# Kernel tuning notes

Hardware: AMD Instinct MI355X
Metric: run time of the kernel (lower is better)

Reference implementation:

```python
import jax, jax.numpy as jnp
import numpy as np

B, N, K = 8, 2048, 32
EPS = 1e-5


def _lrelu(x):
    return jnp.where(x >= 0, x, 0.2 * x)


def _bn(x, p):
    # inference BatchNorm; x: [B, C, ...], p: [4, C] = (gamma, beta, mean, var)
    g, b, m, v = p[0], p[1], p[2], p[3]
    shape = (1, -1) + (1,) * (x.ndim - 2)
    scale = g * jax.lax.rsqrt(v + EPS)
    return (x - m.reshape(shape)) * scale.reshape(shape) + b.reshape(shape)


def _group(x, k):
    # ops.group with xyz_or_feature='feature', feature_or_diff='diff'
    # x: [B, C, N] -> edge features [B, 2C, N, k] = cat(neighbor - center, center)
    xt = jnp.transpose(x, (0, 2, 1))  # [B, N, C]
    sq = jnp.sum(xt * xt, axis=-1)    # [B, N]
    dist = sq[:, :, None] - 2.0 * jnp.einsum('bnc,bmc->bnm', xt, xt) + sq[:, None, :]
    idx = jax.lax.top_k(-dist, k)[1]  # [B, N, k] nearest neighbors
    nbr = jax.vmap(lambda f, i: f[i])(xt, idx)  # [B, N, k, C]
    center = xt[:, :, None, :]
    edge = jnp.concatenate([nbr - center, jnp.broadcast_to(center, nbr.shape)], axis=-1)
    return jnp.transpose(edge, (0, 3, 1, 2))  # [B, 2C, N, k]


def _edgeconv(x, w1, bn1, w2, bn2, k):
    e = _group(x, k)
    h = _lrelu(_bn(jnp.einsum('oc,bcnk->bonk', w1, e), bn1))
    h = _lrelu(_bn(jnp.einsum('oc,bcnk->bonk', w2, h), bn2))
    return jnp.max(h, axis=-1)  # max over neighbors -> [B, C_out, N]


def _model(x,
           ec1_w1, ec1_bn1, ec1_w2, ec1_bn2,
           ec2_w1, ec2_bn1, ec2_w2, ec2_bn2,
           ec3_w1, ec3_bn1, ec3_w2, ec3_bn2,
           emb_w, q_w, k_w, v_w, att_bn1, ff_w1, ff_w2, att_bn2,
           cb_w, cb_bn):
    # EdgeConvBlock (3 stacked EdgeConvs, outputs concatenated)
    f1 = _edgeconv(x, ec1_w1, ec1_bn1, ec1_w2, ec1_bn2, K)
    f2 = _edgeconv(f1, ec2_w1, ec2_bn1, ec2_w2, ec2_bn2, K)
    f3 = _edgeconv(f2, ec3_w1, ec3_bn1, ec3_w2, ec3_bn2, K)
    xc = jnp.concatenate([f1, f2, f3], axis=1)  # [B, 192, N]
    # Point2PointAttentionBlock: embedding then dense self-attention
    h = jnp.einsum('oc,bcn->bon', emb_w, xc)  # [B, 1024, N]
    q = jnp.einsum('oc,bcn->bon', q_w, h)
    kk = jnp.einsum('oc,bcn->bon', k_w, h)
    v = jnp.einsum('oc,bcn->bon', v_w, h)
    scale = jnp.sqrt(jnp.asarray(h.shape[1], h.dtype))
    att = jax.nn.softmax(jnp.einsum('bcn,bcm->bnm', q, kk) / scale, axis=-1)  # [B, N, N]
    x_r = jnp.einsum('bnm,bcm->bcn', att, v)
    h = _bn(h + x_r, att_bn1)
    ff = jnp.einsum('oc,bcn->bon', ff_w2, _lrelu(jnp.einsum('oc,bcn->bon', ff_w1, h)))
    h = _bn(h + ff, att_bn2)
    # ConvBlock head
    return _lrelu(_bn(jnp.einsum('oc,bcn->bon', cb_w, h), cb_bn))  # [B, 1024, N]


def setup_inputs() -> dict:
    key = jax.random.key(0)
    ks = iter(jax.random.split(key, 32))

    def randn(shape, s=0.1):
        return jax.random.normal(next(ks), shape, jnp.float32) * s

    def bnp(c):
        return jax.random.uniform(next(ks), (4, c), jnp.float32, 0.1, 1.0)

    return {
        'x': randn((B, 3, N), 1.0),
        'ec1_w1': randn((64, 6)), 'ec1_bn1': bnp(64),
        'ec1_w2': randn((64, 64)), 'ec1_bn2': bnp(64),
        'ec2_w1': randn((64, 128)), 'ec2_bn1': bnp(64),
        'ec2_w2': randn((64, 64)), 'ec2_bn2': bnp(64),
        'ec3_w1': randn((64, 128)), 'ec3_bn1': bnp(64),
        'ec3_w2': randn((64, 64)), 'ec3_bn2': bnp(64),
        'emb_w': randn((1024, 192), 0.05),
        'q_w': randn((1024, 1024), 0.03),
        'k_w': randn((1024, 1024), 0.03),
        'v_w': randn((1024, 1024), 0.03),
        'att_bn1': bnp(1024),
        'ff_w1': randn((512, 1024), 0.03),
        'ff_w2': randn((1024, 512), 0.03),
        'att_bn2': bnp(1024),
        'cb_w': randn((1024, 1024), 0.03),
        'cb_bn': bnp(1024),
    }


def reference(x,
              ec1_w1, ec1_bn1, ec1_w2, ec1_bn2,
              ec2_w1, ec2_bn1, ec2_w2, ec2_bn2,
              ec3_w1, ec3_bn1, ec3_w2, ec3_bn2,
              emb_w, q_w, k_w, v_w, att_bn1, ff_w1, ff_w2, att_bn2,
              cb_w, cb_bn):
    return _model(x,
                  ec1_w1, ec1_bn1, ec1_w2, ec1_bn2,
                  ec2_w1, ec2_bn1, ec2_w2, ec2_bn2,
                  ec3_w1, ec3_bn1, ec3_w2, ec3_bn2,
                  emb_w, q_w, k_w, v_w, att_bn1, ff_w1, ff_w2, att_bn2,
                  cb_w, cb_bn)
```

## Files before the change

kernel.cpp:

```cpp
#include <hip/hip_runtime.h>
#include <hip/hip_bf16.h>

constexpr int Bn  = 8;
constexpr int Np  = 2048;
constexpr int KNN = 32;

typedef __attribute__((ext_vector_type(8))) short bf16x8;
typedef __attribute__((ext_vector_type(4))) float f32x4;

__device__ static inline void gll16(const void* g, void* l) {
  __builtin_amdgcn_global_load_lds((const __attribute__((address_space(1))) void*)g,
                                   (__attribute__((address_space(3))) void*)l, 16, 0, 0);
}

__device__ static inline unsigned short f2bf(float x) {
  union { __hip_bfloat16 h; unsigned short u; } cv; cv.h = __float2bfloat16(x); return cv.u;
}
__device__ static inline float bf2f(unsigned short u) {
  union { __hip_bfloat16 h; unsigned short u; } cv; cv.u = u; return __bfloat162float(cv.h);
}

__global__ __launch_bounds__(256)
void cvt_bf16_kernel(const float* __restrict__ s, __hip_bfloat16* __restrict__ d, int n) {
  int i = blockIdx.x * 256 + threadIdx.x;
  if (i < n) d[i] = __float2bfloat16(s[i]);
}

template<int CIN, int K1>
__global__ __launch_bounds__(256)
void cvt_w1a(const float* __restrict__ w1, __hip_bfloat16* __restrict__ out) {
  int i = blockIdx.x * 256 + threadIdx.x;
  if (i >= 64 * K1) return;
  int o = i / K1, c = i - o * K1;
  out[i] = __float2bfloat16(c < CIN ? w1[o * 2 * CIN + c] : 0.f);
}

__global__ __launch_bounds__(256)
void xpose_kernel(const float* __restrict__ x, float* __restrict__ xt,
                  __hip_bfloat16* __restrict__ xb) {
  int i = blockIdx.x * 256 + threadIdx.x;
  int b = i >> 11, n = i & 2047;
  const float* p = x + (long)b * 3 * Np + n;
  float vx = p[0], vy = p[Np], vz = p[2 * Np];
  xt[(long)i * 4 + 0] = vx;
  xt[(long)i * 4 + 1] = vy;
  xt[(long)i * 4 + 2] = vz;
  xt[(long)i * 4 + 3] = 0.f;
  __hip_bfloat16* q = xb + (long)i * 8;
  q[0] = __float2bfloat16(vx); q[1] = __float2bfloat16(vy);
  q[2] = __float2bfloat16(vz);
  q[3] = __float2bfloat16(0.f); q[4] = q[3]; q[5] = q[3]; q[6] = q[3]; q[7] = q[3];
}

template<int C, int CP>
__global__ __launch_bounds__(256)
void sq_kernel(const float* __restrict__ f, float* __restrict__ out) {
  int i = blockIdx.x * 256 + threadIdx.x;
  const float* p = f + (long)i * CP;
  float s = 0.f;
#pragma unroll
  for (int c = 0; c < C; ++c) s += p[c] * p[c];
  out[i] = s;
}

template<int CIN, int CP>
__global__ __launch_bounds__(256)
void split_kernel(const float* __restrict__ f, __hip_bfloat16* __restrict__ fhi,
                  __hip_bfloat16* __restrict__ flo) {
  int i = blockIdx.x * 256 + threadIdx.x;
  int n = i >> 6, c = i & 63;
  float v = (c < CIN) ? f[(long)n * CP + c] : 0.f;
  __hip_bfloat16 h = __float2bfloat16(v);
  fhi[i] = h;
  flo[i] = __float2bfloat16(v - __bfloat162float(h));
}

__device__ static inline unsigned umin32(unsigned a, unsigned b) { return a < b ? a : b; }

__device__ static inline unsigned long long shfl64x(unsigned long long k, int m) {
  unsigned lo = (unsigned)__shfl_xor((int)(unsigned)k, m);
  unsigned hi = (unsigned)__shfl_xor((int)(unsigned)(k >> 32), m);
  return ((unsigned long long)hi << 32) | (unsigned long long)lo;
}

__device__ static inline unsigned lane_sort64_u32(unsigned v, int lane) {
#pragma unroll
  for (int k = 2; k <= 64; k <<= 1) {
#pragma unroll
    for (int j = k >> 1; j > 0; j >>= 1) {
      unsigned o = (unsigned)__shfl_xor((int)v, j);
      bool dir = ((lane & k) == 0);
      bool lower = ((lane & j) == 0);
      bool keep = (v < o) == (dir == lower);
      v = keep ? v : o;
    }
  }
  return v;
}

__device__ static inline unsigned long long lane_sort64_u64(unsigned long long v, int lane) {
#pragma unroll
  for (int k = 2; k <= 64; k <<= 1) {
#pragma unroll
    for (int j = k >> 1; j > 0; j >>= 1) {
      unsigned long long o = shfl64x(v, j);
      bool dir = ((lane & k) == 0);
      bool lower = ((lane & j) == 0);
      bool keep = (v < o) == (dir == lower);
      v = keep ? v : o;
    }
  }
  return v;
}

__device__ static inline unsigned long long lane_merge64(unsigned long long a,
                                                         unsigned long long b, int lane) {
  unsigned long long br = shfl64x(b, 63);
  unsigned long long m = a < br ? a : br;
#pragma unroll
  for (int j = 32; j > 0; j >>= 1) {
    unsigned long long o = shfl64x(m, j);
    bool lower = ((lane & j) == 0);
    bool keep = (m < o) == lower;
    m = keep ? m : o;
  }
  return m;
}

template<int MAP, int CAP>
__device__ static inline void row_topk(const unsigned* val, unsigned long long* cbuf,
                                       int lane, int* outp) {
  unsigned tmn[16];
#pragma unroll
  for (int i = 0; i < 16; ++i) tmn[i] = umin32(val[i], val[i + 16]);
#pragma unroll
  for (int w2 = 8; w2 >= 1; w2 >>= 1)
#pragma unroll
    for (int i = 0; i < 8; ++i)
      if (i < w2) tmn[i] = umin32(tmn[i], tmn[i + w2]);

  unsigned T = (unsigned)__shfl((int)lane_sort64_u32(tmn[0], lane), 31);

  int S = 0;
#pragma unroll
  for (int s = 0; s < 32; ++s) {
    bool p = val[s] <= T;
    unsigned long long mask = __ballot(p);
    int pre = __builtin_amdgcn_mbcnt_hi((unsigned)(mask >> 32),
              __builtin_amdgcn_mbcnt_lo((unsigned)mask, 0u));
    int pos = S + pre;
    unsigned idx = (MAP == 0) ? (unsigned)((s >> 2) * 256 + lane * 4 + (s & 3))
                              : (unsigned)((s >> 2) * 256 + (s & 3) * 64 + lane);
    if (p && pos < CAP) cbuf[pos] = ((unsigned long long)val[s] << 32) | idx;
    S += (int)__popcll(mask);
  }

  unsigned long long cur;
  if (S <= CAP) {
    unsigned long long k0 = (lane < S) ? cbuf[lane] : ~0ull;
    cur = lane_sort64_u64(k0, lane);
    for (int c = 64; c < S; c += 64) {
      unsigned long long kc = (c + lane < S) ? cbuf[c + lane] : ~0ull;
      cur = lane_merge64(cur, lane_sort64_u64(kc, lane), lane);
    }
  } else {
    cur = ~0ull;
    for (int s = 0; s < 32; ++s) {
      unsigned idx = (MAP == 0) ? (unsigned)((s >> 2) * 256 + lane * 4 + (s & 3))
                                : (unsigned)((s >> 2) * 256 + (s & 3) * 64 + lane);
      unsigned long long kc = ((unsigned long long)val[s] << 32) | idx;
      cur = lane_merge64(cur, lane_sort64_u64(kc, lane), lane);
    }
  }
  if (lane < KNN) outp[lane] = (int)(unsigned)cur;
}

__global__ __launch_bounds__(512)
void knn3_kernel(const float* __restrict__ xt, const float* __restrict__ sqb,
                 int* __restrict__ idxOut) {
  __shared__ float4 F[2048];
  __shared__ float sqS[2048];
  __shared__ unsigned long long cbuf[8 * 256];
  int t = threadIdx.x, lane = t & 63, w = t >> 6;
  long pb = (long)blockIdx.y * Np;
  for (int e = t; e < 2048; e += 512) {
    F[e] = ((const float4*)xt)[pb + e];
    sqS[e] = sqb[pb + e];
  }
  __syncthreads();
  int row = blockIdx.x * 8 + w;
  float4 a = F[row];
  unsigned val[32];
#pragma unroll
  for (int j4 = 0; j4 < 8; ++j4)
#pragma unroll
    for (int u = 0; u < 4; ++u) {
      int col = j4 * 256 + u * 64 + lane;
      float4 fb = F[col];
      float d = sqS[col] - 2.f * (a.x * fb.x + a.y * fb.y + a.z * fb.z);
      unsigned b = __float_as_uint(d);
      val[j4 * 4 + u] = b ^ ((unsigned)((int)b >> 31) | 0x80000000u);
    }
  row_topk<1, 256>(val, cbuf + w * 256, lane, idxOut + (pb + row) * KNN);
}

__global__ __launch_bounds__(512, 4)
void knn16_kernel(const __hip_bfloat16* __restrict__ fhi,
                  const __hip_bfloat16* __restrict__ flo,
                  const float* __restrict__ sqb, int* __restrict__ idxOut) {
  constexpr int LDW = 2052;
  constexpr int CAP = 224;
  __shared__ __align__(16) float Dw[8 * LDW];
  __shared__ unsigned long long cbuf[8 * CAP];
  int t = threadIdx.x, lane = t & 63, w = t >> 6;
  long pb = (long)blockIdx.y * Np;
  int r0 = blockIdx.x * 8;
  const __hip_bfloat16* fh = fhi + pb * 64;
  const __hip_bfloat16* fl = flo + pb * 64;
  const float* sqg = sqb + pb;

  int ar = r0 + (lane & 7);
  int kc = (lane >> 4) * 8;
  int n15 = lane & 15;
  bf16x8 ah[2], al[2];
#pragma unroll
  for (int k2 = 0; k2 < 2; ++k2) {
    ah[k2] = *(const bf16x8*)(fh + (long)ar * 64 + k2 * 32 + kc);
    al[k2] = *(const bf16x8*)(fl + (long)ar * 64 + k2 * 32 + kc);
  }

  int cb0 = w * 256;
  bf16x8 b0h[2], b0l[2], b1h[2], b1l[2];
  float sq0, sq1;
  {
    int bc = cb0 + n15;
#pragma unroll
    for (int k2 = 0; k2 < 2; ++k2) {
      b0h[k2] = *(const bf16x8*)(fh + (long)bc * 64 + k2 * 32 + kc);
      b0l[k2] = *(const bf16x8*)(fl + (long)bc * 64 + k2 * 32 + kc);
    }
    sq0 = sqg[bc];
    bc = cb0 + 16 + n15;
#pragma unroll
    for (int k2 = 0; k2 < 2; ++k2) {
      b1h[k2] = *(const bf16x8*)(fh + (long)bc * 64 + k2 * 32 + kc);
      b1l[k2] = *(const bf16x8*)(fl + (long)bc * 64 + k2 * 32 + kc);
    }
    sq1 = sqg[bc];
  }
  int m0 = (lane >> 4) * 4;
  bool wr = (lane < 32);
#pragma unroll
  for (int cp = 0; cp < 8; ++cp) {
    {
      int ct = cp * 2;
      bf16x8 nh[2], nl[2]; float nsq = 0.f;
      if (ct + 2 < 16) {
        int bc = cb0 + (ct + 2) * 16 + n15;
#pragma unroll
        for (int k2 = 0; k2 < 2; ++k2) {
          nh[k2] = *(const bf16x8*)(fh + (long)bc * 64 + k2 * 32 + kc);
          nl[k2] = *(const bf16x8*)(fl + (long)bc * 64 + k2 * 32 + kc);
        }
        nsq = sqg[bc];
      }
      f32x4 acc = f32x4{0.f, 0.f, 0.f, 0.f};
#pragma unroll
      for (int k2 = 0; k2 < 2; ++k2) {
        acc = __builtin_amdgcn_mfma_f32_16x16x32_bf16(ah[k2], b0h[k2], acc, 0, 0, 0);
        acc = __builtin_amdgcn_mfma_f32_16x16x32_bf16(ah[k2], b0l[k2], acc, 0, 0, 0);
        acc = __builtin_amdgcn_mfma_f32_16x16x32_bf16(al[k2], b0h[k2], acc, 0, 0, 0);
      }
      if (wr) {
        int col = cb0 + ct * 16 + n15;
#pragma unroll
        for (int r = 0; r < 4; ++r)
          Dw[(m0 + r) * LDW + col] = sq0 - 2.f * acc[r];
      }
#pragma unroll
      for (int k2 = 0; k2 < 2; ++k2) { b0h[k2] = nh[k2]; b0l[k2] = nl[k2]; }
      sq0 = nsq;
    }
    {
      int ct = cp * 2 + 1;
      bf16x8 nh[2], nl[2]; float nsq = 0.f;
      if (ct + 2 < 16) {
        int bc = cb0 + (ct + 2) * 16 + n15;
#pragma unroll
        for (int k2 = 0; k2 < 2; ++k2) {
          nh[k2] = *(const bf16x8*)(fh + (long)bc * 64 + k2 * 32 + kc);
          nl[k2] = *(const bf16x8*)(fl + (long)bc * 64 + k2 * 32 + kc);
        }
        nsq = sqg[bc];
      }
      f32x4 acc = f32x4{0.f, 0.f, 0.f, 0.f};
#pragma unroll
      for (int k2 = 0; k2 < 2; ++k2) {
        acc = __builtin_amdgcn_mfma_f32_16x16x32_bf16(ah[k2], b1h[k2], acc, 0, 0, 0);
        acc = __builtin_amdgcn_mfma_f32_16x16x32_bf16(ah[k2], b1l[k2], acc, 0, 0, 0);
        acc = __builtin_amdgcn_mfma_f32_16x16x32_bf16(al[k2], b1h[k2], acc, 0, 0, 0);
      }
      if (wr) {
        int col = cb0 + ct * 16 + n15;
#pragma unroll
        for (int r = 0; r < 4; ++r)
          Dw[(m0 + r) * LDW + col] = sq1 - 2.f * acc[r];
      }
#pragma unroll
      for (int k2 = 0; k2 < 2; ++k2) { b1h[k2] = nh[k2]; b1l[k2] = nl[k2]; }
      sq1 = nsq;
    }
  }
  __syncthreads();

  {
    unsigned val[32];
    const float4* rp = (const float4*)&Dw[w * LDW];
#pragma unroll
    for (int j4 = 0; j4 < 8; ++j4) {
      float4 f4 = rp[j4 * 64 + lane];
      float fv[4] = {f4.x, f4.y, f4.z, f4.w};
#pragma unroll
      for (int u = 0; u < 4; ++u) {
        unsigned b = __float_as_uint(fv[u]);
        val[j4 * 4 + u] = b ^ ((unsigned)((int)b >> 31) | 0x80000000u);
      }
    }
    row_topk<0, CAP>(val, cbuf + w * CAP, lane, idxOut + (pb + r0 + w) * KNN);
  }
}

template<int CIN, int CP>
__global__ __launch_bounds__(256)
void biasker(const float* __restrict__ feat, const float* __restrict__ w1,
             float* __restrict__ bias) {
  __shared__ float wd[64][CIN + 1];
  int tid = threadIdx.x;
  for (int e = tid; e < 64 * CIN; e += 256) {
    int o = e / CIN, c = e - o * CIN;
    wd[o][c] = w1[o * 2 * CIN + CIN + c] - w1[o * 2 * CIN + c];
  }
  __syncthreads();
  int wv = tid >> 6, o = tid & 63;
  float wr_[CIN];
#pragma unroll
  for (int c = 0; c < CIN; ++c) wr_[c] = wd[o][c];
  long base = (long)blockIdx.y * Np + blockIdx.x * 32 + wv * 8;
  for (int p = 0; p < 8; ++p) {
    const float* fr = feat + (base + p) * CP;
    float acc = 0.f;
#pragma unroll
    for (int c = 0; c < CIN; ++c) acc = fmaf(wr_[c], fr[c], acc);
    bias[(base + p) * 64 + o] = acc;
  }
}

template<int K1>
__global__ __launch_bounds__(256)
void edge_mfma(const __hip_bfloat16* __restrict__ featb, int fstride,
               const int* __restrict__ idx, const float* __restrict__ bias,
               const __hip_bfloat16* __restrict__ w1b,
               const __hip_bfloat16* __restrict__ w2b,
               const float* __restrict__ bn1, const float* __restrict__ bn2,
               float* __restrict__ fout, __hip_bfloat16* __restrict__ xcseg) {
  __shared__ __align__(16) char lds[32768 + 64 * K1 * 2 + 8192 + 1024 + 512];
  __hip_bfloat16* A  = (__hip_bfloat16*)lds;
  __hip_bfloat16* H1 = A + 128 * K1;
  float*          H2 = (float*)lds;
  __hip_bfloat16* W1 = (__hip_bfloat16*)(lds + 32768);
  __hip_bfloat16* W2 = W1 + 64 * K1;
  float* biasS = (float*)(lds + 32768 + 64 * K1 * 2 + 8192);
  int*   idxS  = (int*)(biasS + 256);

  int t = threadIdx.x, lane = t & 63, w = t >> 6;
  long pb = (long)blockIdx.y * Np;
  int p0 = blockIdx.x * 4;

  if (t < 128) idxS[t] = idx[(pb + p0 + (t >> 5)) * KNN + (t & 31)];
  biasS[w * 64 + lane] = bias[(pb + p0 + w) * 64 + lane];
  for (int e = t; e < 64 * K1 / 8; e += 256)
    ((ulonglong2*)W1)[e] = ((const ulonglong2*)w1b)[e];
  for (int e = t; e < 512; e += 256)
    ((ulonglong2*)W2)[e] = ((const ulonglong2*)w2b)[e];
  __syncthreads();

  if (K1 == 64) {
#pragma unroll
    for (int i = 0; i < 4; ++i) {
      int e = t + i * 256;
      int r = e >> 3, cc = e & 7;
      const ulonglong2* src = (const ulonglong2*)(featb + (pb + idxS[r]) * fstride) + cc;
      ((ulonglong2*)(A + r * 64))[cc] = *src;
    }
  } else {
    if (t < 128) {
      int r = t;
      ulonglong2 z; z.x = 0; z.y = 0;
      ((ulonglong2*)(A + r * 32))[0] = *(const ulonglong2*)(featb + (pb + idxS[r]) * fstride);
      ((ulonglong2*)(A + r * 32))[1] = z;
      ((ulonglong2*)(A + r * 32))[2] = z;
      ((ulonglong2*)(A + r * 32))[3] = z;
    }
  }

  int ocol = lane & 15;
  float sc1[4], sh1[4], sc2[4], sh2[4];
#pragma unroll
  for (int jn = 0; jn < 4; ++jn) {
    int o = jn * 16 + ocol;
    sc1[jn] = bn1[o] * rsqrtf(bn1[192 + o] + 1e-5f);
    sh1[jn] = bn1[64 + o] - bn1[128 + o] * sc1[jn];
    sc2[jn] = bn2[o] * rsqrtf(bn2[192 + o] + 1e-5f);
    sh2[jn] = bn2[64 + o] - bn2[128 + o] * sc2[jn];
  }
  __syncthreads();

  int mrow = lane & 15;
  int kc   = (lane >> 4) * 8;
  constexpr int KS = K1 / 32;

  f32x4 acc[2][4];
#pragma unroll
  for (int im = 0; im < 2; ++im)
#pragma unroll
    for (int jn = 0; jn < 4; ++jn) acc[im][jn] = f32x4{0.f, 0.f, 0.f, 0.f};
#pragma unroll
  for (int s = 0; s < KS; ++s) {
    bf16x8 af[2], bf_[4];
#pragma unroll
    for (int im = 0; im < 2; ++im)
      af[im] = *(const bf16x8*)(A + (w * 32 + im * 16 + mrow) * K1 + s * 32 + kc);
#pragma unroll
    for (int jn = 0; jn < 4; ++jn)
      bf_[jn] = *(const bf16x8*)(W1 + (jn * 16 + mrow) * K1 + s * 32 + kc);
#pragma unroll
    for (int im = 0; im < 2; ++im)
#pragma unroll
      for (int jn = 0; jn < 4; ++jn)
        acc[im][jn] = __builtin_amdgcn_mfma_f32_16x16x32_bf16(af[im], bf_[jn], acc[im][jn], 0, 0, 0);
  }
#pragma unroll
  for (int im = 0; im < 2; ++im)
#pragma unroll
    for (int jn = 0; jn < 4; ++jn) {
      int o = jn * 16 + ocol;
      float bsv = biasS[w * 64 + o];
#pragma unroll
      for (int r = 0; r < 4; ++r) {
        int m = w * 32 + im * 16 + (lane >> 4) * 4 + r;
        float x = (acc[im][jn][r] + bsv) * sc1[jn] + sh1[jn];
        x = fmaxf(x, 0.2f * x);
        H1[m * 64 + o] = __float2bfloat16(x);
      }
    }
  __syncthreads();

  bf16x8 a2[2][2], b2[4][2];
#pragma unroll
  for (int im = 0; im < 2; ++im)
#pragma unroll
    for (int s = 0; s < 2; ++s)
      a2[im][s] = *(const bf16x8*)(H1 + (w * 32 + im * 16 + mrow) * 64 + s * 32 + kc);
#pragma unroll
  for (int jn = 0; jn < 4; ++jn)
#pragma unroll
    for (int s = 0; s < 2; ++s)
      b2[jn][s] = *(const bf16x8*)(W2 + (jn * 16 + mrow) * 64 + s * 32 + kc);
  __syncthreads();

  f32x4 acc2[2][4];
#pragma unroll
  for (int im = 0; im < 2; ++im)
#pragma unroll
    for (int jn = 0; jn < 4; ++jn) acc2[im][jn] = f32x4{0.f, 0.f, 0.f, 0.f};
#pragma unroll
  for (int s = 0; s < 2; ++s)
#pragma unroll
    for (int im = 0; im < 2; ++im)
#pragma unroll
      for (int jn = 0; jn < 4; ++jn)
        acc2[im][jn] = __builtin_amdgcn_mfma_f32_16x16x32_bf16(a2[im][s], b2[jn][s], acc2[im][jn], 0, 0, 0);
#pragma unroll
  for (int im = 0; im < 2; ++im)
#pragma unroll
    for (int jn = 0; jn < 4; ++jn) {
      int o = jn * 16 + ocol;
#pragma unroll
      for (int r = 0; r < 4; ++r) {
        int m = w * 32 + im * 16 + (lane >> 4) * 4 + r;
        float x = acc2[im][jn][r] * sc2[jn] + sh2[jn];
        x = fmaxf(x, 0.2f * x);
        H2[m * 64 + o] = x;
      }
    }
  __syncthreads();

  {
    int o = t & 63;
    float m = -3.4e38f;
#pragma unroll
    for (int k = 0; k < 32; ++k) m = fmaxf(m, H2[(w * 32 + k) * 64 + o]);
    int n2 = p0 + w;
    if (fout) fout[(pb + n2) * 64 + o] = m;
    xcseg[(pb + n2) * 192 + o] = __float2bfloat16(m);
  }
}

template<int OUTF, int BNMODE, int RESID, int LRELU>
__global__ __launch_bounds__(512)
void gemm_db(const __hip_bfloat16* __restrict__ A, int lda, long sA,
             const __hip_bfloat16* __restrict__ B, int ldb, long sB,
             void* __restrict__ Cv, int ldc, long sC,
             const __hip_bfloat16* __restrict__ R, long sR,
             const float* __restrict__ bn, int bnlen, int Kd,
             int gx, int gy) {
  int nwg = gx * gy * Bn;
  int cpx = nwg >> 3;
  int orig = blockIdx.x;
  int wg = (orig & 7) * cpx + (orig >> 3);
  int bz = wg / (gx * gy);
  int rem = wg - bz * (gx * gy);
  int by = rem / gx;
  int bx = rem - by * gx;
  A += (long)bz * sA;
  B += (long)bz * sB;
  long i0 = (long)bx * 256, j0 = (long)by * 256;

  __shared__ __hip_bfloat16 As[2][256 * 64];
  __shared__ __hip_bfloat16 Bs[2][256 * 64];

  int t = threadIdx.x, lane = t & 63, w = t >> 6;
  int wm = w & 1, wn = w >> 1;

  f32x4 acc[8][4];
#pragma unroll
  for (int im = 0; im < 8; ++im)
#pragma unroll
    for (int jn = 0; jn < 4; ++jn) acc[im][jn] = f32x4{0.f, 0.f, 0.f, 0.f};

#define STAGE_DB(bi, kt)                                                     \
  {                                                                          \
    _Pragma("unroll")                                                        \
    for (int i = 0; i < 4; ++i) {                                            \
      int e = t + i * 512;                                                   \
      int r = e >> 3, c = e & 7;                                             \
      int cs = c ^ (r & 7);                                                  \
      gll16(A + (i0 + r) * lda + (kt) * 64 + cs * 8,                         \
            (__hip_bfloat16*)As[bi] + e * 8);                                \
    }                                                                        \
    _Pragma("unroll")                                                        \
    for (int i = 0; i < 4; ++i) {                                            \
      int e = t + i * 512;                                                   \
      int r = e >> 3, c = e & 7;                                             \
      int cs = c ^ (r & 7);                                                  \
      gll16(B + (j0 + r) * ldb + (kt) * 64 + cs * 8,                         \
            (__hip_bfloat16*)Bs[bi] + e * 8);                                \
    }                                                                        \
  }

  int nt = Kd >> 6;
  STAGE_DB(0, 0);
  __syncthreads();

  int cur = 0;
  for (int kt = 0; kt < nt; ++kt) {
    if (kt + 1 < nt) STAGE_DB(cur ^ 1, kt + 1);
    const __hip_bfloat16* Ab = As[cur];
    const __hip_bfloat16* Bb = Bs[cur];
#pragma unroll
    for (int ks = 0; ks < 2; ++ks) {
      bf16x8 af[8], bfv[4];
#pragma unroll
      for (int im = 0; im < 8; ++im) {
        int ra = wm * 128 + im * 16 + (lane & 15);
        int q = (ks * 4 + (lane >> 4)) ^ (ra & 7);
        af[im] = *(const bf16x8*)(Ab + ra * 64 + q * 8);
      }
#pragma unroll
      for (int jn = 0; jn < 4; ++jn) {
        int rb = wn * 64 + jn * 16 + (lane & 15);
        int q = (ks * 4 + (lane >> 4)) ^ (rb & 7);
        bfv[jn] = *(const bf16x8*)(Bb + rb * 64 + q * 8);
      }
#pragma unroll
      for (int im = 0; im < 8; ++im)
#pragma unroll
        for (int jn = 0; jn < 4; ++jn)
          acc[im][jn] = __builtin_amdgcn_mfma_f32_16x16x32_bf16(af[im], bfv[jn], acc[im][jn], 0, 0, 0);
    }
    __syncthreads();
    cur ^= 1;
  }
#undef STAGE_DB

  int mlocal = (lane >> 4) * 4;
  int nlocal = lane & 15;
#pragma unroll
  for (int i = 0; i < 8; ++i) {
    long m0 = i0 + wm * 128 + i * 16 + mlocal;
    float bsc[4], bsh[4];
    if (BNMODE == 1) {
#pragma unroll
      for (int r = 0; r < 4; ++r) {
        long c = m0 + r;
        float sc = bn[c] * rsqrtf(bn[3 * bnlen + c] + 1e-5f);
        bsc[r] = sc;
        bsh[r] = bn[bnlen + c] - bn[2 * bnlen + c] * sc;
      }
    }
#pragma unroll
    for (int j = 0; j < 4; ++j) {
      long nn = j0 + wn * 64 + j * 16 + nlocal;
      float sc2 = 1.f, sh2 = 0.f;
      if (BNMODE == 2) {
        sc2 = bn[nn] * rsqrtf(bn[3 * bnlen + nn] + 1e-5f);
        sh2 = bn[bnlen + nn] - bn[2 * bnlen + nn] * sc2;
      }
      f32x4 v = acc[i][j];
      float o4[4];
      ushort4 rv;
      if (RESID) rv = *(const ushort4*)(R + (long)bz * sR + nn * ldc + m0);
#pragma unroll
      for (int r = 0; r < 4; ++r) {
        float x = v[r];
        if (RESID) x += bf2f(r == 0 ? rv.x : r == 1 ? rv.y : r == 2 ? rv.z : rv.w);
        if (BNMODE == 1) x = x * bsc[r] + bsh[r];
        if (BNMODE == 2) x = x * sc2 + sh2;
        if (LRELU) x = (x >= 0.f) ? x : 0.2f * x;
        o4[r] = x;
      }
      if (OUTF) {
        float* Cp = (float*)Cv + (long)bz * sC + nn * ldc + m0;
        *(float4*)Cp = make_float4(o4[0], o4[1], o4[2], o4[3]);
      } else {
        __hip_bfloat16* Cp = (__hip_bfloat16*)Cv + (long)bz * sC + nn * ldc + m0;
        ushort4 sv;
        sv.x = f2bf(o4[0]); sv.y = f2bf(o4[1]); sv.z = f2bf(o4[2]); sv.w = f2bf(o4[3]);
        *(ushort4*)Cp = sv;
      }
    }
  }
}

__global__ __launch_bounds__(256)
void softmax_bf(__hip_bfloat16* __restrict__ S) {
  long row = (long)blockIdx.y * Np + blockIdx.x;
  __hip_bfloat16* p = S + row * Np;
  int t = threadIdx.x;
  const float scale = 0.03125f;
  float v[8];
  float mx = -3.4e38f;
#pragma unroll
  for (int u = 0; u < 8; ++u) {
    v[u] = __bfloat162float(p[u * 256 + t]) * scale;
    mx = fmaxf(mx, v[u]);
  }
  __shared__ float red[4];
#pragma unroll
  for (int off = 32; off > 0; off >>= 1) mx = fmaxf(mx, __shfl_xor(mx, off));
  if ((t & 63) == 0) red[t >> 6] = mx;
  __syncthreads();
  mx = fmaxf(fmaxf(red[0], red[1]), fmaxf(red[2], red[3]));
  __syncthreads();
  float sum = 0.f;
#pragma unroll
  for (int u = 0; u < 8; ++u) { v[u] = __expf(v[u] - mx); sum += v[u]; }
#pragma unroll
  for (int off = 32; off > 0; off >>= 1) sum += __shfl_xor(sum, off);
  if ((t & 63) == 0) red[t >> 6] = sum;
  __syncthreads();
  sum = red[0] + red[1] + red[2] + red[3];
  float inv = 1.f / sum;
#pragma unroll
  for (int u = 0; u < 8; ++u) p[u * 256 + t] = __float2bfloat16(v[u] * inv);
}

extern "C" void kernel_launch(void* const* d_in, const int* in_sizes, int n_in,
                              void* d_out, int out_size, void* d_ws, size_t ws_size,
                              hipStream_t stream) {
  const float* x       = (const float*)d_in[0];
  const float* ec1_w1  = (const float*)d_in[1];
  const float* ec1_bn1 = (const float*)d_in[2];
  const float* ec1_w2  = (const float*)d_in[3];
  const float* ec1_bn2 = (const float*)d_in[4];
  const float* ec2_w1  = (const float*)d_in[5];
  const float* ec2_bn1 = (const float*)d_in[6];
  const float* ec2_w2  = (const float*)d_in[7];
  const float* ec2_bn2 = (const float*)d_in[8];
  const float* ec3_w1  = (const float*)d_in[9];
  const float* ec3_bn1 = (const float*)d_in[10];
  const float* ec3_w2  = (const float*)d_in[11];
  const float* ec3_bn2 = (const float*)d_in[12];
  const float* emb_w   = (const float*)d_in[13];
  const float* q_w     = (const float*)d_in[14];
  const float* k_w     = (const float*)d_in[15];
  const float* v_w     = (const float*)d_in[16];
  const float* att_bn1 = (const float*)d_in[17];
  const float* ff_w1   = (const float*)d_in[18];
  const float* ff_w2   = (const float*)d_in[19];
  const float* att_bn2 = (const float*)d_in[20];
  const float* cb_w    = (const float*)d_in[21];
  const float* cb_bn   = (const float*)d_in[22];
  float* out = (float*)d_out;
  (void)in_sizes; (void)n_in; (void)out_size; (void)ws_size;

  float* ws  = (float*)d_ws;
  float* xt  = ws;
  float* f1  = xt + 65536;
  float* f2  = f1 + 1048576;
  float* sqb = f2 + 1048576;
  int*   idxb = (int*)(sqb + 16384);
  __hip_bfloat16* xc  = (__hip_bfloat16*)(idxb + 524288);
  __hip_bfloat16* wts = xc + 3145728;
  __hip_bfloat16* ew  = wts + 5439488;
  __hip_bfloat16* xb  = ew + 22528;
  float* big = (float*)(xb + 131072);
  __hip_bfloat16* hb  = (__hip_bfloat16*)big;
  __hip_bfloat16* qb  = hb + 16777216;
  __hip_bfloat16* kb  = qb + 16777216;
  __hip_bfloat16* vtb = kb + 16777216;
  __hip_bfloat16* Sb  = vtb + 16777216;
  __hip_bfloat16* fhi = (__hip_bfloat16*)big;
  __hip_bfloat16* flo = fhi + 1048576;
  float* biasb = big + 33554432;

  __hip_bfloat16* emb_wb = wts;
  __hip_bfloat16* q_wb   = wts + 196608;
  __hip_bfloat16* k_wb   = wts + 1245184;
  __hip_bfloat16* v_wb   = wts + 2293760;
  __hip_bfloat16* ff1_wb = wts + 3342336;
  __hip_bfloat16* ff2_wb = wts + 3866624;
  __hip_bfloat16* cb_wb  = wts + 4390912;

  __hip_bfloat16* w1a1_b = ew;
  __hip_bfloat16* w2_1b  = ew + 2048;
  __hip_bfloat16* w1a2_b = ew + 6144;
  __hip_bfloat16* w2_2b  = ew + 10240;
  __hip_bfloat16* w1a3_b = ew + 14336;
  __hip_bfloat16* w2_3b  = ew + 18432;

  const long sN1024 = (long)Np * 1024;
  const long sN512  = (long)Np * 512;
  const long sN192  = (long)Np * 192;
  const long sNN    = (long)Np * Np;

  cvt_bf16_kernel<<<768,  256, 0, stream>>>(emb_w, emb_wb, 196608);
  cvt_bf16_kernel<<<4096, 256, 0, stream>>>(q_w,   q_wb,   1048576);
  cvt_bf16_kernel<<<4096, 256, 0, stream>>>(k_w,   k_wb,   1048576);
  cvt_bf16_kernel<<<4096, 256, 0, stream>>>(v_w,   v_wb,   1048576);
  cvt_bf16_kernel<<<2048, 256, 0, stream>>>(ff_w1, ff1_wb, 524288);
  cvt_bf16_kernel<<<2048, 256, 0, stream>>>(ff_w2, ff2_wb, 524288);
  cvt_bf16_kernel<<<4096, 256, 0, stream>>>(cb_w,  cb_wb,  1048576);
  cvt_w1a<3, 32><<<8, 256, 0, stream>>>(ec1_w1, w1a1_b);
  cvt_w1a<64, 64><<<16, 256, 0, stream>>>(ec2_w1, w1a2_b);
  cvt_w1a<64, 64><<<16, 256, 0, stream>>>(ec3_w1, w1a3_b);
  cvt_bf16_kernel<<<16, 256, 0, stream>>>(ec1_w2, w2_1b, 4096);
  cvt_bf16_kernel<<<16, 256, 0, stream>>>(ec2_w2, w2_2b, 4096);
  cvt_bf16_kernel<<<16, 256, 0, stream>>>(ec3_w2, w2_3b, 4096);

  xpose_kernel<<<64, 256, 0, stream>>>(x, xt, xb);

  sq_kernel<3, 4><<<64, 256, 0, stream>>>(xt, sqb);
  knn3_kernel<<<dim3(Np / 8, Bn), 512, 0, stream>>>(xt, sqb, idxb);
  biasker<3, 4><<<dim3(Np / 32, Bn), 256, 0, stream>>>(xt, ec1_w1, biasb);
  edge_mfma<32><<<dim3(Np / 4, Bn), 256, 0, stream>>>(
      xb, 8, idxb, biasb, w1a1_b, w2_1b, ec1_bn1, ec1_bn2, f1, xc);

  sq_kernel<64, 64><<<64, 256, 0, stream>>>(f1, sqb);
  split_kernel<64, 64><<<4096, 256, 0, stream>>>(f1, fhi, flo);
  knn16_kernel<<<dim3(Np / 8, Bn), 512, 0, stream>>>(fhi, flo, sqb, idxb);
  biasker<64, 64><<<dim3(Np / 32, Bn), 256, 0, stream>>>(f1, ec2_w1, biasb);
  edge_mfma<64><<<dim3(Np / 4, Bn), 256, 0, stream>>>(
      xc, 192, idxb, biasb, w1a2_b, w2_2b, ec2_bn1, ec2_bn2, f2, xc + 64);

  sq_kernel<64, 64><<<64, 256, 0, stream>>>(f2, sqb);
  split_kernel<64, 64><<<4096, 256, 0, stream>>>(f2, fhi, flo);
  knn16_kernel<<<dim3(Np / 8, Bn), 512, 0, stream>>>(fhi, flo, sqb, idxb);
  biasker<64, 64><<<dim3(Np / 32, Bn), 256, 0, stream>>>(f2, ec3_w1, biasb);
  edge_mfma<64><<<dim3(Np / 4, Bn), 256, 0, stream>>>(
      xc + 64, 192, idxb, biasb, w1a3_b, w2_3b, ec3_bn1, ec3_bn2, nullptr, xc + 128);

  gemm_db<0, 0, 0, 0><<<dim3(4 * 8 * Bn), 512, 0, stream>>>(
      emb_wb, 192, 0, xc, 192, sN192, hb, 1024, sN1024, nullptr, 0, nullptr, 0, 192, 4, 8);

  gemm_db<0, 0, 0, 0><<<dim3(4 * 8 * Bn), 512, 0, stream>>>(
      q_wb, 1024, 0, hb, 1024, sN1024, qb, 1024, sN1024, nullptr, 0, nullptr, 0, 1024, 4, 8);
  gemm_db<0, 0, 0, 0><<<dim3(4 * 8 * Bn), 512, 0, stream>>>(
      k_wb, 1024, 0, hb, 1024, sN1024, kb, 1024, sN1024, nullptr, 0, nullptr, 0, 1024, 4, 8);
  gemm_db<0, 0, 0, 0><<<dim3(8 * 4 * Bn), 512, 0, stream>>>(
      hb, 1024, sN1024, v_wb, 1024, 0, vtb, 2048, sN1024, nullptr, 0, nullptr, 0, 1024, 8, 4);

  gemm_db<0, 0, 0, 0><<<dim3(8 * 8 * Bn), 512, 0, stream>>>(
      kb, 1024, sN1024, qb, 1024, sN1024, Sb, 2048, sNN, nullptr, 0, nullptr, 0, 1024, 8, 8);
  softmax_bf<<<dim3(Np, Bn), 256, 0, stream>>>(Sb);

  gemm_db<0, 1, 1, 0><<<dim3(4 * 8 * Bn), 512, 0, stream>>>(
      vtb, 2048, sN1024, Sb, 2048, sNN, hb, 1024, sN1024, hb, sN1024, att_bn1, 1024, 2048, 4, 8);

  gemm_db<0, 0, 0, 1><<<dim3(2 * 8 * Bn), 512, 0, stream>>>(
      ff1_wb, 1024, 0, hb, 1024, sN1024, qb, 512, sN512, nullptr, 0, nullptr, 0, 1024, 2, 8);
  gemm_db<0, 1, 1, 0><<<dim3(4 * 8 * Bn), 512, 0, stream>>>(
      ff2_wb, 512, 0, qb, 512, sN512, hb, 1024, sN1024, hb, sN1024, att_bn2, 1024, 512, 4, 8);

  gemm_db<1, 2, 0, 1><<<dim3(8 * 4 * Bn), 512, 0, stream>>>(
      hb, 1024, sN1024, cb_wb, 1024, 0, out, 2048, sN1024, nullptr, 0, cb_bn, 1024, 1024, 8, 4);
}
```

Before: 1.012 ms.

## Replace bitonic top-k sorts with radix-select and double kNN rows per block

Swaps the bitonic sort used to find the 32nd-smallest threshold and the final candidate sort for a bitwise radix-select that uses wave ballots and popcounts. The selected indices are written unsorted through mbcnt compaction. The knn16 kernel now handles 16 rows per block instead of 8, so all MFMA output lanes are used, and it stages the squared norms in LDS instead of loading them per column. Risks include the changed output order of neighbor indices, if downstream code depends on it, plus larger LDS use and lower occupancy in knn16.

```diff
diff --git a/kernel.cpp b/kernel.cpp
--- a/kernel.cpp
+++ b/kernel.cpp
@@ -77,25 +77,15 @@
 
 __device__ static inline unsigned umin32(unsigned a, unsigned b) { return a < b ? a : b; }
 
+__device__ static inline int mbcnt64(unsigned long long m) {
+  return __builtin_amdgcn_mbcnt_hi((unsigned)(m >> 32),
+         __builtin_amdgcn_mbcnt_lo((unsigned)m, 0u));
+}
+
 __device__ static inline unsigned long long shfl64x(unsigned long long k, int m) {
   unsigned lo = (unsigned)__shfl_xor((int)(unsigned)k, m);
   unsigned hi = (unsigned)__shfl_xor((int)(unsigned)(k >> 32), m);
   return ((unsigned long long)hi << 32) | (unsigned long long)lo;
-}
-
-__device__ static inline unsigned lane_sort64_u32(unsigned v, int lane) {
-#pragma unroll
-  for (int k = 2; k <= 64; k <<= 1) {
-#pragma unroll
-    for (int j = k >> 1; j > 0; j >>= 1) {
-      unsigned o = (unsigned)__shfl_xor((int)v, j);
-      bool dir = ((lane & k) == 0);
-      bool lower = ((lane & j) == 0);
-      bool keep = (v < o) == (dir == lower);
-      v = keep ? v : o;
-    }
-  }
-  return v;
 }
 
 __device__ static inline unsigned long long lane_sort64_u64(unsigned long long v, int lane) {
@@ -127,6 +117,16 @@
   return m;
 }
 
+__device__ static inline unsigned kth_u32(unsigned v, int km1) {
+  unsigned p = 0;
+#pragma unroll
+  for (int b = 31; b >= 0; --b) {
+    unsigned t = p | (1u << b);
+    if ((int)__popcll(__ballot(v < t)) <= km1) p = t;
+  }
+  return p;
+}
+
 template<int MAP, int CAP>
 __device__ static inline void row_topk(const unsigned* val, unsigned long long* cbuf,
                                        int lane, int* outp) {
@@ -139,40 +139,81 @@
     for (int i = 0; i < 8; ++i)
       if (i < w2) tmn[i] = umin32(tmn[i], tmn[i + w2]);
 
-  unsigned T = (unsigned)__shfl((int)lane_sort64_u32(tmn[0], lane), 31);
+  unsigned T = kth_u32(tmn[0], 31);
 
   int S = 0;
 #pragma unroll
   for (int s = 0; s < 32; ++s) {
     bool p = val[s] <= T;
     unsigned long long mask = __ballot(p);
-    int pre = __builtin_amdgcn_mbcnt_hi((unsigned)(mask >> 32),
-              __builtin_amdgcn_mbcnt_lo((unsigned)mask, 0u));
-    int pos = S + pre;
+    int pos = S + mbcnt64(mask);
     unsigned idx = (MAP == 0) ? (unsigned)((s >> 2) * 256 + lane * 4 + (s & 3))
                               : (unsigned)((s >> 2) * 256 + (s & 3) * 64 + lane);
     if (p && pos < CAP) cbuf[pos] = ((unsigned long long)val[s] << 32) | idx;
     S += (int)__popcll(mask);
   }
 
-  unsigned long long cur;
-  if (S <= CAP) {
-    unsigned long long k0 = (lane < S) ? cbuf[lane] : ~0ull;
-    cur = lane_sort64_u64(k0, lane);
-    for (int c = 64; c < S; c += 64) {
-      unsigned long long kc = (c + lane < S) ? cbuf[c + lane] : ~0ull;
-      cur = lane_merge64(cur, lane_sort64_u64(kc, lane), lane);
+  if (S <= 64) {
+    unsigned long long k = (lane < S) ? cbuf[lane] : ~0ull;
+    unsigned vs = (unsigned)(k >> 32), ix = (unsigned)k;
+    unsigned vstar = kth_u32(vs, 31);
+    int c1 = (int)__popcll(__ballot(vs < vstar));
+    int r = 32 - c1;
+    unsigned istar = 0;
+#pragma unroll
+    for (int b = 10; b >= 0; --b) {
+      unsigned t = istar | (1u << b);
+      if ((int)__popcll(__ballot(vs == vstar && ix < t)) <= r - 1) istar = t;
+    }
+    bool sel = (vs < vstar) || (vs == vstar && ix <= istar);
+    unsigned long long m = __ballot(sel);
+    if (sel) outp[mbcnt64(m)] = (int)ix;
+  } else if (S <= CAP) {
+    int nslot = (S + 63) >> 6;
+    unsigned vs[CAP / 64], is_[CAP / 64];
+#pragma unroll
+    for (int q = 0; q < CAP / 64; ++q) {
+      unsigned long long k = (q * 64 + lane < S) ? cbuf[q * 64 + lane] : ~0ull;
+      vs[q] = (unsigned)(k >> 32);
+      is_[q] = (unsigned)k;
+    }
+    unsigned vstar = 0;
+#pragma unroll
+    for (int b = 31; b >= 0; --b) {
+      unsigned t = vstar | (1u << b);
+      int c = 0;
+      for (int q = 0; q < nslot; ++q) c += (int)__popcll(__ballot(vs[q] < t));
+      if (c <= 31) vstar = t;
+    }
+    int c1 = 0;
+    for (int q = 0; q < nslot; ++q) c1 += (int)__popcll(__ballot(vs[q] < vstar));
+    int r = 32 - c1;
+    unsigned istar = 0;
+#pragma unroll
+    for (int b = 10; b >= 0; --b) {
+      unsigned t = istar | (1u << b);
+      int c = 0;
+      for (int q = 0; q < nslot; ++q)
+        c += (int)__popcll(__ballot(vs[q] == vstar && is_[q] < t));
+      if (c <= r - 1) istar = t;
+    }
+    int base = 0;
+    for (int q = 0; q < nslot; ++q) {
+      bool sel = (vs[q] < vstar) || (vs[q] == vstar && is_[q] <= istar);
+      unsigned long long m = __ballot(sel);
+      if (sel) outp[base + mbcnt64(m)] = (int)is_[q];
+      base += (int)__popcll(m);
     }
   } else {
-    cur = ~0ull;
+    unsigned long long cur = ~0ull;
     for (int s = 0; s < 32; ++s) {
       unsigned idx = (MAP == 0) ? (unsigned)((s >> 2) * 256 + lane * 4 + (s & 3))
                                 : (unsigned)((s >> 2) * 256 + (s & 3) * 64 + lane);
       unsigned long long kc = ((unsigned long long)val[s] << 32) | idx;
       cur = lane_merge64(cur, lane_sort64_u64(kc, lane), lane);
     }
-  }
-  if (lane < KNN) outp[lane] = (int)(unsigned)cur;
+    if (lane < KNN) outp[lane] = (int)(unsigned)cur;
+  }
 }
 
 __global__ __launch_bounds__(512)
@@ -204,22 +245,24 @@
   row_topk<1, 256>(val, cbuf + w * 256, lane, idxOut + (pb + row) * KNN);
 }
 
-__global__ __launch_bounds__(512, 4)
+__global__ __launch_bounds__(512)
 void knn16_kernel(const __hip_bfloat16* __restrict__ fhi,
                   const __hip_bfloat16* __restrict__ flo,
                   const float* __restrict__ sqb, int* __restrict__ idxOut) {
   constexpr int LDW = 2052;
-  constexpr int CAP = 224;
-  __shared__ __align__(16) float Dw[8 * LDW];
+  constexpr int CAP = 256;
+  __shared__ __align__(16) float Dw[16 * LDW];
+  __shared__ float sqS[2048];
   __shared__ unsigned long long cbuf[8 * CAP];
   int t = threadIdx.x, lane = t & 63, w = t >> 6;
   long pb = (long)blockIdx.y * Np;
-  int r0 = blockIdx.x * 8;
+  int r0 = blockIdx.x * 16;
   const __hip_bfloat16* fh = fhi + pb * 64;
   const __hip_bfloat16* fl = flo + pb * 64;
-  const float* sqg = sqb + pb;
-
-  int ar = r0 + (lane & 7);
+
+  ((float4*)sqS)[t] = ((const float4*)(sqb + pb))[t];
+
+  int ar = r0 + (lane & 15);
   int kc = (lane >> 4) * 8;
   int n15 = lane & 15;
   bf16x8 ah[2], al[2];
@@ -228,10 +271,10 @@
     ah[k2] = *(const bf16x8*)(fh + (long)ar * 64 + k2 * 32 + kc);
     al[k2] = *(const bf16x8*)(fl + (long)ar * 64 + k2 * 32 + kc);
   }
+  __syncthreads();
 
   int cb0 = w * 256;
   bf16x8 b0h[2], b0l[2], b1h[2], b1l[2];
-  float sq0, sq1;
   {
     int bc = cb0 + n15;
 #pragma unroll
@@ -239,22 +282,19 @@
       b0h[k2] = *(const bf16x8*)(fh + (long)bc * 64 + k2 * 32 + kc);
       b0l[k2] = *(const bf16x8*)(fl + (long)bc * 64 + k2 * 32 + kc);
     }
-    sq0 = sqg[bc];
     bc = cb0 + 16 + n15;
 #pragma unroll
     for (int k2 = 0; k2 < 2; ++k2) {
       b1h[k2] = *(const bf16x8*)(fh + (long)bc * 64 + k2 * 32 + kc);
       b1l[k2] = *(const bf16x8*)(fl + (long)bc * 64 + k2 * 32 + kc);
     }
-    sq1 = sqg[bc];
   }
   int m0 = (lane >> 4) * 4;
-  bool wr = (lane < 32);
 #pragma unroll
   for (int cp = 0; cp < 8; ++cp) {
     {
       int ct = cp * 2;
-      bf16x8 nh[2], nl[2]; float nsq = 0.f;
+      bf16x8 nh[2], nl[2];
       if (ct + 2 < 16) {
         int bc = cb0 + (ct + 2) * 16 + n15;
 #pragma unroll
@@ -262,7 +302,6 @@
           nh[k2] = *(const bf16x8*)(fh + (long)bc * 64 + k2 * 32 + kc);
           nl[k2] = *(const bf16x8*)(fl + (long)bc * 64 + k2 * 32 + kc);
         }
-        nsq = sqg[bc];
       }
       f32x4 acc = f32x4{0.f, 0.f, 0.f, 0.f};
 #pragma unroll
@@ -271,19 +310,17 @@
         acc = __builtin_amdgcn_mfma_f32_16x16x32_bf16(ah[k2], b0l[k2], acc, 0, 0, 0);
         acc = __builtin_amdgcn_mfma_f32_16x16x32_bf16(al[k2], b0h[k2], acc, 0, 0, 0);
       }
-      if (wr) {
-        int col = cb0 + ct * 16 + n15;
-#pragma unroll
-        for (int r = 0; r < 4; ++r)
-          Dw[(m0 + r) * LDW + col] = sq0 - 2.f * acc[r];
-      }
+      int col = cb0 + ct * 16 + n15;
+      float sqv = sqS[col];
+#pragma unroll
+      for (int r = 0; r < 4; ++r)
+        Dw[(m0 + r) * LDW + col] = sqv - 2.f * acc[r];
 #pragma unroll
       for (int k2 = 0; k2 < 2; ++k2) { b0h[k2] = nh[k2]; b0l[k2] = nl[k2]; }
-      sq0 = nsq;
     }
     {
       int ct = cp * 2 + 1;
-      bf16x8 nh[2], nl[2]; float nsq = 0.f;
+      bf16x8 nh[2], nl[2];
       if (ct + 2 < 16) {
         int bc = cb0 + (ct + 2) * 16 + n15;
 #pragma unroll
@@ -291,7 +328,6 @@
           nh[k2] = *(const bf16x8*)(fh + (long)bc * 64 + k2 * 32 + kc);
           nl[k2] = *(const bf16x8*)(fl + (long)bc * 64 + k2 * 32 + kc);
         }
-        nsq = sqg[bc];
       }
       f32x4 acc = f32x4{0.f, 0.f, 0.f, 0.f};
 #pragma unroll
@@ -300,22 +336,21 @@
         acc = __builtin_amdgcn_mfma_f32_16x16x32_bf16(ah[k2], b1l[k2], acc, 0, 0, 0);
         acc = __builtin_amdgcn_mfma_f32_16x16x32_bf16(al[k2], b1h[k2], acc, 0, 0, 0);
       }
-      if (wr) {
-        int col = cb0 + ct * 16 + n15;
-#pragma unroll
-        for (int r = 0; r < 4; ++r)
-          Dw[(m0 + r) * LDW + col] = sq1 - 2.f * acc[r];
-      }
+      int col = cb0 + ct * 16 + n15;
+      float sqv = sqS[col];
+#pragma unroll
+      for (int r = 0; r < 4; ++r)
+        Dw[(m0 + r) * LDW + col] = sqv - 2.f * acc[r];
 #pragma unroll
       for (int k2 = 0; k2 < 2; ++k2) { b1h[k2] = nh[k2]; b1l[k2] = nl[k2]; }
-      sq1 = nsq;
-    }
-  }
-  __syncthreads();
-
-  {
+    }
+  }
+  __syncthreads();
+
+  for (int rr = 0; rr < 2; ++rr) {
+    int row = w * 2 + rr;
     unsigned val[32];
-    const float4* rp = (const float4*)&Dw[w * LDW];
+    const float4* rp = (const float4*)&Dw[row * LDW];
 #pragma unroll
     for (int j4 = 0; j4 < 8; ++j4) {
       float4 f4 = rp[j4 * 64 + lane];
@@ -326,7 +361,7 @@
         val[j4 * 4 + u] = b ^ ((unsigned)((int)b >> 31) | 0x80000000u);
       }
     }
-    row_topk<0, CAP>(val, cbuf + w * CAP, lane, idxOut + (pb + r0 + w) * KNN);
+    row_topk<0, CAP>(val, cbuf + w * CAP, lane, idxOut + (pb + r0 + row) * KNN);
   }
 }
 
@@ -768,14 +803,14 @@
 
   sq_kernel<64, 64><<<64, 256, 0, stream>>>(f1, sqb);
   split_kernel<64, 64><<<4096, 256, 0, stream>>>(f1, fhi, flo);
-  knn16_kernel<<<dim3(Np / 8, Bn), 512, 0, stream>>>(fhi, flo, sqb, idxb);
+  knn16_kernel<<<dim3(Np / 16, Bn), 512, 0, stream>>>(fhi, flo, sqb, idxb);
   biasker<64, 64><<<dim3(Np / 32, Bn), 256, 0, stream>>>(f1, ec2_w1, biasb);
   edge_mfma<64><<<dim3(Np / 4, Bn), 256, 0, stream>>>(
       xc, 192, idxb, biasb, w1a2_b, w2_2b, ec2_bn1, ec2_bn2, f2, xc + 64);
 
   sq_kernel<64, 64><<<64, 256, 0, stream>>>(f2, sqb);
   split_kernel<64, 64><<<4096, 256, 0, stream>>>(f2, fhi, flo);
-  knn16_kernel<<<dim3(Np / 8, Bn), 512, 0, stream>>>(fhi, flo, sqb, idxb);
+  knn16_kernel<<<dim3(Np / 16, Bn), 512, 0, stream>>>(fhi, flo, sqb, idxb);
   biasker<64, 64><<<dim3(Np / 32, Bn), 256, 0, stream>>>(f2, ec3_w1, biasb);
   edge_mfma<64><<<dim3(Np / 4, Bn), 256, 0, stream>>>(
       xc + 64, 192, idxb, biasb, w1a3_b, w2_3b, ec3_bn1, ec3_bn2, nullptr, xc + 128);
```

New measurement: 947.6 us. 1.07x faster.
